# Optimization experiments

Hardware: AMD Instinct MI355X
Metric: run time of the kernel (lower is better)

Reference implementation:

```python
import jax, jax.numpy as jnp
import numpy as np

B, N, C, H = 4, 1024, 768, 12
D = C // H  # head_dim = 64


def setup_inputs() -> dict:
    key = jax.random.key(0)
    ks = jax.random.split(key, 16)
    def lin(k, fan_in, fan_out):
        # torch Linear init: U(-1/sqrt(fan_in), 1/sqrt(fan_in)); stored as [in, out]
        bound = 1.0 / np.sqrt(fan_in)
        kw, kb = jax.random.split(k)
        W = jax.random.uniform(kw, (fan_in, fan_out), minval=-bound, maxval=bound, dtype=jnp.float32)
        b = jax.random.uniform(kb, (fan_out,), minval=-bound, maxval=bound, dtype=jnp.float32)
        return W, b
    Wq, bq = lin(ks[0], C, C)
    Wk, bk = lin(ks[1], C, C)
    Wv, bv = lin(ks[2], C, C)
    Wo, bo = lin(ks[3], C, C)
    Wd1, bd1 = lin(ks[4], 1, 16)
    Wd2, bd2 = lin(ks[5], 16, H)
    x = jax.random.normal(ks[6], (B, N, C), dtype=jnp.float32)
    coords = jax.random.uniform(ks[7], (B, N, 2), dtype=jnp.float32)
    return {"x": x, "coords": coords,
            "Wq": Wq, "bq": bq, "Wk": Wk, "bk": bk, "Wv": Wv, "bv": bv,
            "Wo": Wo, "bo": bo, "Wd1": Wd1, "bd1": bd1, "Wd2": Wd2, "bd2": bd2}


def reference(x, coords, Wq, bq, Wk, bk, Wv, bv, Wo, bo, Wd1, bd1, Wd2, bd2):
    scale = D ** (-0.5)
    # projections -> [B, H, N, D]
    def heads(t):
        return t.reshape(B, N, H, D).transpose(0, 2, 1, 3)
    q = heads(x @ Wq + bq)
    k = heads(x @ Wk + bk)
    v = heads(x @ Wv + bv)
    # content scores [B, H, N, N]
    content = jnp.einsum('bhid,bhjd->bhij', q, k) * scale
    # pairwise distances [B, N, N, 1]
    diff = coords[:, :, None, :] - coords[:, None, :, :]
    dist = jnp.sqrt(jnp.sum(diff * diff, axis=-1, keepdims=True) + 1e-6)
    # distance MLP: 1 -> 16 -> H, then permute to [B, H, N, N]
    hbias = jax.nn.relu(dist @ Wd1 + bd1)
    spatial = (hbias @ Wd2 + bd2).transpose(0, 3, 1, 2)
    attn = jax.nn.softmax(content + spatial, axis=-1)
    out = jnp.einsum('bhij,bhjd->bhid', attn, v)
    out = out.transpose(0, 2, 1, 3).reshape(B, N, C)
    out = out @ Wo + bo
    return out, attn
```

## Files before the change

kernel.cpp:

```cpp
#include <hip/hip_runtime.h>
#include <cstddef>
#include <cstdint>

#define Bc 4
#define Nc 1024
#define Cc 768
#define Hc 12
#define Dc 64
#define BHc 48
#define QKV_ELEMS ((size_t)Bc * Nc * Cc)

typedef __attribute__((ext_vector_type(4))) unsigned int u32x4;
typedef __attribute__((ext_vector_type(2))) unsigned int u32x2;
typedef __attribute__((ext_vector_type(8))) short s16x8;
typedef __attribute__((ext_vector_type(8))) _Float16 h16x8;
typedef __attribute__((ext_vector_type(4))) float fx4;
typedef __attribute__((ext_vector_type(2))) float fx2;

union Frag { u32x4 u; s16x8 s; h16x8 f16; unsigned short h[8]; };

__device__ inline unsigned short f2bf(float x) {
    union { float f; uint32_t u; } c; c.f = x;
    return (unsigned short)((c.u + 0x7FFFu + ((c.u >> 16) & 1u)) >> 16);
}
__device__ inline float bf2f(unsigned short b) {
    union { uint32_t u; float f; } c; c.u = ((uint32_t)b) << 16;
    return c.f;
}
__device__ inline void split8(const float* v, u32x4& hi, u32x4& lo) {
    Frag fh, fl;
    #pragma unroll
    for (int e = 0; e < 8; ++e) {
        const unsigned short hb = f2bf(v[e]);
        fh.h[e] = hb;
        fl.h[e] = f2bf(v[e] - bf2f(hb));
    }
    hi = fh.u; lo = fl.u;
}
__device__ inline void split8h(const float* v, u32x4& hi, u32x4& lo) {
    Frag fh, fl;
    #pragma unroll
    for (int e = 0; e < 8; ++e) {
        const _Float16 hb = (_Float16)v[e];
        fh.f16[e] = hb;
        fl.f16[e] = (_Float16)(v[e] - (float)hb);
    }
    hi = fh.u; lo = fl.u;
}

__global__ __launch_bounds__(256) void prep_w_kernel(
    const float* __restrict__ Wq, const float* __restrict__ Wk,
    const float* __restrict__ Wv, const float* __restrict__ Wo,
    unsigned short* __restrict__ Thi, unsigned short* __restrict__ Tlo)
{
    __shared__ float scr[64 * 65];
    const int mat = blockIdx.z;
    const float* W = (mat == 0) ? Wq : (mat == 1) ? Wk : (mat == 2) ? Wv : Wo;
    const int k0 = blockIdx.y * 64, n0 = blockIdx.x * 64;
    const int tid = threadIdx.x;

    #pragma unroll
    for (int it = 0; it < 4; ++it) {
        const int lin = tid + it * 256;
        const int r = lin >> 4, c4 = (lin & 15) << 2;
        const fx4 v = *(const fx4*)&W[(size_t)(k0 + r) * 768 + n0 + c4];
        scr[r * 65 + c4 + 0] = v[0]; scr[r * 65 + c4 + 1] = v[1];
        scr[r * 65 + c4 + 2] = v[2]; scr[r * 65 + c4 + 3] = v[3];
    }
    __syncthreads();
    unsigned short* th = Thi + (size_t)mat * 768 * 768;
    unsigned short* tl = Tlo + (size_t)mat * 768 * 768;
    #pragma unroll
    for (int it = 0; it < 16; ++it) {
        const int lin = tid + it * 256;
        const int n = lin >> 6, kq = lin & 63;
        const float val = scr[kq * 65 + n];
        const size_t o = (size_t)(n0 + n) * 768 + k0 + kq;
        const unsigned short hb = f2bf(val);
        th[o] = hb;
        tl[o] = f2bf(val - bf2f(hb));
    }
}

__global__ __launch_bounds__(256) void prep_tables_kernel(
    const float* __restrict__ Wd1, const float* __restrict__ bd1,
    const float* __restrict__ Wd2, const float* __restrict__ bd2,
    float* __restrict__ abPack, unsigned char* __restrict__ lut)
{
    __shared__ float w1s[16], b1s[16], kn[16];
    __shared__ int rank[16];
    const int tid = threadIdx.x;
    if (tid < 16) {
        const float w1 = Wd1[tid], b1 = bd1[tid];
        w1s[tid] = w1; b1s[tid] = b1;
        kn[tid] = (w1 != 0.0f) ? (-b1 / w1) : INFINITY;
    }
    __syncthreads();
    if (tid < 16) {
        int rk = 0;
        for (int u = 0; u < 16; ++u) {
            const float ku = kn[u], km = kn[tid];
            if (ku < km || (ku == km && u < tid)) ++rk;
        }
        rank[tid] = rk;
    }
    __syncthreads();
    if (tid < 17 * 12) {
        const int s = tid / 12, h = tid % 12;
        float a = 0.0f, be = bd2[h];
        for (int u = 0; u < 16; ++u) {
            const float w1 = w1s[u], b1 = b1s[u];
            bool act;
            if (w1 > 0.0f)      act = (rank[u] < s);
            else if (w1 < 0.0f) act = (rank[u] >= s);
            else                act = (b1 > 0.0f);
            if (act) {
                const float w2 = Wd2[u * 12 + h];
                a  += w2 * w1;
                be += w2 * b1;
            }
        }
        abPack[tid * 2 + 0] = a;
        abPack[tid * 2 + 1] = be;
    }
    for (int b = tid; b < 2048; b += 256) {
        const float rep = (b + 0.5f) * (1.41422f / 2048.0f);
        int cnt = 0;
        for (int t = 0; t < 16; ++t) cnt += (rep > kn[t]) ? 1 : 0;
        lut[b] = (unsigned char)cnt;
    }
}

__global__ __launch_bounds__(256) void split_x_kernel(
    const float* __restrict__ x, unsigned short* __restrict__ xhi,
    unsigned short* __restrict__ xlo)
{
    const size_t t = (size_t)blockIdx.x * 256 + threadIdx.x;
    float vv[8];
    const fx4 a = *(const fx4*)&x[t * 8];
    const fx4 b = *(const fx4*)&x[t * 8 + 4];
    vv[0]=a[0]; vv[1]=a[1]; vv[2]=a[2]; vv[3]=a[3];
    vv[4]=b[0]; vv[5]=b[1]; vv[6]=b[2]; vv[7]=b[3];
    u32x4 hi, lo; split8(vv, hi, lo);
    *(u32x4*)&xhi[t * 8] = hi;
    *(u32x4*)&xlo[t * 8] = lo;
}

struct SmemG { u32x4 ah[512]; u32x4 al[512]; u32x4 bh[512]; u32x4 bl[512]; };
struct SmemT { float scr[64 * 68]; };
union SmemU { SmemG g; SmemT t; };

template<int OMODE>
__global__ __launch_bounds__(256) void gemm_mfma_kernel(
    const unsigned short* __restrict__ Ahi, const unsigned short* __restrict__ Alo,
    const unsigned short* __restrict__ Bhi, const unsigned short* __restrict__ Blo,
    const float* __restrict__ bias,
    float* __restrict__ outF,
    unsigned short* __restrict__ Ohi, unsigned short* __restrict__ Olo)
{
    __shared__ SmemU sm;
    const int tid = threadIdx.x;
    const int w = tid >> 6, L = tid & 63;
    const int Lr = L & 15, Lg = L >> 4;
    const int m0 = blockIdx.y * 64, n0 = blockIdx.x * 64;

    fx4 acc[2][2] = {};

    for (int kk = 0; kk < 768; kk += 64) {
        #pragma unroll
        for (int it = 0; it < 2; ++it) {
            const int slot = tid + it * 256;
            const int s = slot >> 6, l = slot & 63;
            const int row = m0 + ((s >> 1) << 4) + (l & 15);
            const int kb = kk + ((s & 1) << 5) + ((l >> 4) << 3);
            sm.g.ah[slot] = *(const u32x4*)&Ahi[(size_t)row * 768 + kb];
            sm.g.al[slot] = *(const u32x4*)&Alo[(size_t)row * 768 + kb];
            const int col = n0 + ((s >> 1) << 4) + (l & 15);
            sm.g.bh[slot] = *(const u32x4*)&Bhi[(size_t)col * 768 + kb];
            sm.g.bl[slot] = *(const u32x4*)&Blo[(size_t)col * 768 + kb];
        }
        __syncthreads();
        #pragma unroll
        for (int kc = 0; kc < 2; ++kc) {
            Frag ah[2], al[2], bh[2], bl[2];
            #pragma unroll
            for (int mm = 0; mm < 2; ++mm) {
                const int rg = (w >> 1) * 2 + mm;
                ah[mm].u = sm.g.ah[(rg * 2 + kc) * 64 + L];
                al[mm].u = sm.g.al[(rg * 2 + kc) * 64 + L];
            }
            #pragma unroll
            for (int nn = 0; nn < 2; ++nn) {
                const int cg = (w & 1) * 2 + nn;
                bh[nn].u = sm.g.bh[(cg * 2 + kc) * 64 + L];
                bl[nn].u = sm.g.bl[(cg * 2 + kc) * 64 + L];
            }
            #pragma unroll
            for (int mm = 0; mm < 2; ++mm)
                #pragma unroll
                for (int nn = 0; nn < 2; ++nn) {
                    acc[mm][nn] = __builtin_amdgcn_mfma_f32_16x16x32_bf16(ah[mm].s, bh[nn].s, acc[mm][nn], 0, 0, 0);
                    acc[mm][nn] = __builtin_amdgcn_mfma_f32_16x16x32_bf16(ah[mm].s, bl[nn].s, acc[mm][nn], 0, 0, 0);
                    acc[mm][nn] = __builtin_amdgcn_mfma_f32_16x16x32_bf16(al[mm].s, bh[nn].s, acc[mm][nn], 0, 0, 0);
                }
        }
        __syncthreads();
    }

    #pragma unroll
    for (int mm = 0; mm < 2; ++mm) {
        const int rl = (w >> 1) * 32 + mm * 16 + Lg * 4;
        #pragma unroll
        for (int nn = 0; nn < 2; ++nn) {
            const int cl = (w & 1) * 32 + nn * 16 + Lr;
            const float bs = bias[n0 + cl];
            #pragma unroll
            for (int r = 0; r < 4; ++r)
                sm.t.scr[(rl + r) * 68 + cl] = acc[mm][nn][r] + bs;
        }
    }
    __syncthreads();

    if (OMODE == 0) {
        const int h = n0 >> 6;
        #pragma unroll
        for (int it = 0; it < 2; ++it) {
            const int t = tid + it * 256;
            const int r = t >> 3, d0 = (t & 7) << 3;
            float vv[8];
            #pragma unroll
            for (int e = 0; e < 8; ++e) vv[e] = sm.t.scr[r * 68 + d0 + e];
            u32x4 hi, lo; split8(vv, hi, lo);
            const int rg = m0 + r, b = rg >> 10, nloc = rg & 1023;
            const size_t o = (((size_t)(b * Hc + h) * Nc + nloc) << 6) + d0;
            *(u32x4*)&Ohi[o] = hi;
            *(u32x4*)&Olo[o] = lo;
        }
    } else if (OMODE == 1) {
        const int b = m0 >> 10, h = n0 >> 6, nbase = m0 & 1023;
        #pragma unroll
        for (int it = 0; it < 2; ++it) {
            const int t = tid + it * 256;
            const int dd = t >> 3, j0 = (t & 7) << 3;
            float vv[8];
            #pragma unroll
            for (int e = 0; e < 8; ++e) vv[e] = sm.t.scr[(j0 + e) * 68 + dd];
            u32x4 hi, lo; split8h(vv, hi, lo);
            const size_t o = (size_t)((b * Hc + h) * Dc + dd) * Nc + nbase + j0;
            *(u32x4*)&Ohi[o] = hi;
            *(u32x4*)&Olo[o] = lo;
        }
    } else {
        #pragma unroll
        for (int it = 0; it < 4; ++it) {
            const int lin = tid + it * 256;
            const int r = lin >> 4, c4 = (lin & 15) << 2;
            const fx4 v = *(const fx4*)&sm.t.scr[r * 68 + c4];
            *(fx4*)&outF[(size_t)(m0 + r) * 768 + n0 + c4] = v;
        }
    }
}

union PvSmem {
    struct { u32x4 vh[512]; u32x4 vl[512]; } v;
    float scr[64 * 68];
};

__global__ __launch_bounds__(256) void attn_fused_kernel(
    const unsigned short* __restrict__ qhi, const unsigned short* __restrict__ qlo,
    const unsigned short* __restrict__ khi, const unsigned short* __restrict__ klo,
    const unsigned short* __restrict__ vThi, const unsigned short* __restrict__ vTlo,
    const float* __restrict__ coords,
    const float* __restrict__ abPack, const unsigned char* __restrict__ lutg,
    float* __restrict__ attn,
    unsigned short* __restrict__ Hphi, unsigned short* __restrict__ Hplo)
{
    __shared__ PvSmem sm;
    __shared__ char escr[4 * 2048];
    __shared__ fx2 cjs[1024];
    __shared__ unsigned char luts[2048];
    __shared__ fx2 abt[17];

    const int tid = threadIdx.x;
    const int w = tid >> 6, L = tid & 63;
    const int Lr = L & 15, Lg = L >> 4;
    const int bh = blockIdx.y, b = bh / Hc, h = bh % Hc;
    const int i0 = blockIdx.x * 64;
    const int i = i0 + w * 16 + Lr;
    const int Lg4 = Lg * 4;

    if (tid < 17) abt[tid] = ((const fx2*)abPack)[tid * Hc + h];
    #pragma unroll
    for (int t = tid; t < 512; t += 256)
        ((uint32_t*)luts)[t] = ((const uint32_t*)lutg)[t];
    #pragma unroll
    for (int t = tid; t < 1024; t += 256)
        cjs[t] = *(const fx2*)&coords[((size_t)b * Nc + t) * 2];

    Frag qh[2], ql[2];
    #pragma unroll
    for (int kc = 0; kc < 2; ++kc) {
        const size_t o = ((size_t)bh * Nc + i) * 64 + kc * 32 + Lg * 8;
        qh[kc].u = *(const u32x4*)&qhi[o];
        ql[kc].u = *(const u32x4*)&qlo[o];
    }
    const fx2 ci = *(const fx2*)&coords[((size_t)b * Nc + i) * 2];
    __syncthreads();

    Frag ef[16][2];
    float m_t[16];
    float m_r = -INFINITY, l_r = 0.f;

    #pragma unroll
    for (int jt = 0; jt < 16; ++jt) {
        const int jbase = jt * 64;

        fx4 acc[4] = {};
        #pragma unroll
        for (int kc = 0; kc < 2; ++kc) {
            Frag kh[4], kl[4];
            #pragma unroll
            for (int cg = 0; cg < 4; ++cg) {
                const size_t o = ((size_t)bh * Nc + jbase + cg * 16 + Lr) * 64 + kc * 32 + Lg * 8;
                kh[cg].u = *(const u32x4*)&khi[o];
                kl[cg].u = *(const u32x4*)&klo[o];
            }
            #pragma unroll
            for (int cg = 0; cg < 4; ++cg) {
                acc[cg] = __builtin_amdgcn_mfma_f32_16x16x32_bf16(kh[cg].s, qh[kc].s, acc[cg], 0, 0, 0);
                acc[cg] = __builtin_amdgcn_mfma_f32_16x16x32_bf16(kl[cg].s, qh[kc].s, acc[cg], 0, 0, 0);
                acc[cg] = __builtin_amdgcn_mfma_f32_16x16x32_bf16(kh[cg].s, ql[kc].s, acc[cg], 0, 0, 0);
            }
        }

        float sv[16];
        #pragma unroll
        for (int cg = 0; cg < 4; ++cg) {
            #pragma unroll
            for (int r = 0; r < 4; ++r) {
                const fx2 cj = cjs[jbase + cg * 16 + Lg4 + r];
                const float dx = ci[0] - cj[0], dy = ci[1] - cj[1];
                const float dist = sqrtf(fmaf(dx, dx, fmaf(dy, dy, 1e-6f)));
                int bin = (int)(dist * (2048.0f / 1.41422f));
                bin = (bin > 2047) ? 2047 : bin;
                const fx2 ab = abt[luts[bin]];
                sv[cg * 4 + r] = fmaf(acc[cg][r], 0.125f, fmaf(ab[0], dist, ab[1]));
            }
        }

        float tm = sv[0];
        #pragma unroll
        for (int e = 1; e < 16; ++e) tm = fmaxf(tm, sv[e]);
        tm = fmaxf(tm, __shfl_xor(tm, 16));
        tm = fmaxf(tm, __shfl_xor(tm, 32));
        m_t[jt] = tm;

        float ts = 0.f;
        #pragma unroll
        for (int e = 0; e < 16; ++e) { sv[e] = __expf(sv[e] - tm); ts += sv[e]; }
        ts += __shfl_xor(ts, 16);
        ts += __shfl_xor(ts, 32);

        #pragma unroll
        for (int p = 0; p < 2; ++p) {
            Frag f;
            #pragma unroll
            for (int r = 0; r < 4; ++r) {
                f.f16[r]     = (_Float16)sv[(2 * p) * 4 + r];
                f.f16[4 + r] = (_Float16)sv[(2 * p + 1) * 4 + r];
            }
            ef[jt][p] = f;
        }

        const float mnew = fmaxf(m_r, tm);
        l_r = l_r * __expf(m_r - mnew) + ts * __expf(tm - mnew);
        m_r = mnew;
    }

    const float m_row = m_r;
    const float il = 1.0f / l_r;

    char* ebase = escr + w * 2048;
    fx4 oacc[4] = {};
    const size_t arow = ((size_t)bh * Nc + i) * Nc;

    #pragma unroll
    for (int jt = 0; jt < 16; ++jt) {
        const int jbase = jt * 64;
        #pragma unroll
        for (int it = 0; it < 2; ++it) {
            const int s = tid + it * 256;
            const int l = s & 63;
            const int dd = ((s >> 7) << 4) + (l & 15);
            const int jo = jbase + ((s >> 6) & 1) * 32 + ((l >> 4) << 3);
            const size_t off = ((size_t)bh * Dc + dd) * Nc + jo;
            sm.v.vh[s] = *(const u32x4*)&vThi[off];
            sm.v.vl[s] = *(const u32x4*)&vTlo[off];
        }

        #pragma unroll
        for (int p = 0; p < 2; ++p) {
            const Frag f = ef[jt][p];
            u32x2 lo2, hi2;
            lo2[0] = f.u[0]; lo2[1] = f.u[1];
            hi2[0] = f.u[2]; hi2[1] = f.u[3];
            const int j0 = (2 * p) * 16 + Lg4;
            const int j1 = (2 * p + 1) * 16 + Lg4;
            *(u32x2*)(ebase + ((Lr * 128 + j0 * 2) ^ ((Lr & 7) << 4))) = lo2;
            *(u32x2*)(ebase + ((Lr * 128 + j1 * 2) ^ ((Lr & 7) << 4))) = hi2;
        }
        __syncthreads();

        const float fscale = __expf(m_t[jt] - m_row) * il;
        const _Float16 fh = (_Float16)fscale;

        #pragma unroll
        for (int kc = 0; kc < 2; ++kc) {
            Frag eA;
            eA.u = *(u32x4*)(ebase + ((Lr * 128 + (kc * 32 + Lg * 8) * 2) ^ ((Lr & 7) << 4)));
            float pf[8];
            #pragma unroll
            for (int e = 0; e < 8; ++e) pf[e] = (float)eA.f16[e] * fscale;
            fx4 w0, w1;
            w0[0]=pf[0]; w0[1]=pf[1]; w0[2]=pf[2]; w0[3]=pf[3];
            w1[0]=pf[4]; w1[1]=pf[5]; w1[2]=pf[6]; w1[3]=pf[7];
            float* ap = &attn[arow + jbase + kc * 32 + Lg * 8];
            *(fx4*)ap = w0;
            *(fx4*)(ap + 4) = w1;
            Frag pa;
            pa.f16 = eA.f16 * fh;
            #pragma unroll
            for (int dg = 0; dg < 4; ++dg) {
                Frag vh, vl;
                vh.u = sm.v.vh[(dg * 2 + kc) * 64 + L];
                vl.u = sm.v.vl[(dg * 2 + kc) * 64 + L];
                oacc[dg] = __builtin_amdgcn_mfma_f32_16x16x32_f16(pa.f16, vh.f16, oacc[dg], 0, 0, 0);
                oacc[dg] = __builtin_amdgcn_mfma_f32_16x16x32_f16(pa.f16, vl.f16, oacc[dg], 0, 0, 0);
            }
        }
        __syncthreads();
    }

    #pragma unroll
    for (int dg = 0; dg < 4; ++dg)
        #pragma unroll
        for (int r = 0; r < 4; ++r)
            sm.scr[(w * 16 + Lg * 4 + r) * 68 + dg * 16 + Lr] = oacc[dg][r];
    __syncthreads();

    #pragma unroll
    for (int it = 0; it < 2; ++it) {
        const int lin = tid + it * 256;
        const int row = lin >> 3, d0 = (lin & 7) << 3;
        float vv[8];
        #pragma unroll
        for (int e = 0; e < 8; ++e) vv[e] = sm.scr[row * 68 + d0 + e];
        u32x4 hi, lo; split8(vv, hi, lo);
        const size_t o = ((size_t)b * Nc + i0 + row) * Cc + h * Dc + d0;
        *(u32x4*)&Hphi[o] = hi;
        *(u32x4*)&Hplo[o] = lo;
    }
}

extern "C" void kernel_launch(void* const* d_in, const int* in_sizes, int n_in,
                              void* d_out, int out_size, void* d_ws, size_t ws_size,
                              hipStream_t stream)
{
    (void)in_sizes; (void)n_in; (void)out_size; (void)ws_size;

    const float* x      = (const float*)d_in[0];
    const float* coords = (const float*)d_in[1];
    const float* Wq = (const float*)d_in[2];  const float* bq = (const float*)d_in[3];
    const float* Wk = (const float*)d_in[4];  const float* bk = (const float*)d_in[5];
    const float* Wv = (const float*)d_in[6];  const float* bv = (const float*)d_in[7];
    const float* Wo = (const float*)d_in[8];  const float* bo = (const float*)d_in[9];
    const float* Wd1 = (const float*)d_in[10]; const float* bd1 = (const float*)d_in[11];
    const float* Wd2 = (const float*)d_in[12]; const float* bd2 = (const float*)d_in[13];

    float* out_main = (float*)d_out;
    float* attn     = out_main + QKV_ELEMS;

    uint8_t* wsb = (uint8_t*)d_ws;
    const size_t SZ_BF = (size_t)BHc * Nc * Dc * 2;
    const size_t SZ_W4 = (size_t)4 * 768 * 768 * 2;
    unsigned short* qhi  = (unsigned short*)(wsb + 0 * SZ_BF);
    unsigned short* qlo  = (unsigned short*)(wsb + 1 * SZ_BF);
    unsigned short* khi  = (unsigned short*)(wsb + 2 * SZ_BF);
    unsigned short* klo  = (unsigned short*)(wsb + 3 * SZ_BF);
    unsigned short* vThi = (unsigned short*)(wsb + 4 * SZ_BF);
    unsigned short* vTlo = (unsigned short*)(wsb + 5 * SZ_BF);
    unsigned short* xhi  = (unsigned short*)(wsb + 6 * SZ_BF);
    unsigned short* xlo  = (unsigned short*)(wsb + 7 * SZ_BF);
    unsigned short* Thi  = (unsigned short*)(wsb + 8 * SZ_BF);
    unsigned short* Tlo  = (unsigned short*)(wsb + 8 * SZ_BF + SZ_W4);
    float* abPack = (float*)(wsb + 8 * SZ_BF + 2 * SZ_W4);
    unsigned char* lut = (unsigned char*)(abPack + 17 * 12 * 2);

    prep_w_kernel<<<dim3(12, 12, 4), 256, 0, stream>>>(Wq, Wk, Wv, Wo, Thi, Tlo);
    prep_tables_kernel<<<1, 256, 0, stream>>>(Wd1, bd1, Wd2, bd2, abPack, lut);
    split_x_kernel<<<dim3(1536), 256, 0, stream>>>(x, xhi, xlo);

    dim3 gGemm(12, 64);
    gemm_mfma_kernel<0><<<gGemm, 256, 0, stream>>>(
        xhi, xlo, Thi + (size_t)0 * 768 * 768, Tlo + (size_t)0 * 768 * 768,
        bq, nullptr, qhi, qlo);
    gemm_mfma_kernel<0><<<gGemm, 256, 0, stream>>>(
        xhi, xlo, Thi + (size_t)1 * 768 * 768, Tlo + (size_t)1 * 768 * 768,
        bk, nullptr, khi, klo);
    gemm_mfma_kernel<1><<<gGemm, 256, 0, stream>>>(
        xhi, xlo, Thi + (size_t)2 * 768 * 768, Tlo + (size_t)2 * 768 * 768,
        bv, nullptr, vThi, vTlo);

    attn_fused_kernel<<<dim3(16, 48), 256, 0, stream>>>(
        qhi, qlo, khi, klo, vThi, vTlo, coords, abPack, lut,
        attn, xhi, xlo);

    gemm_mfma_kernel<2><<<gGemm, 256, 0, stream>>>(
        xhi, xlo, Thi + (size_t)3 * 768 * 768, Tlo + (size_t)3 * 768 * 768,
        bo, out_main, nullptr, nullptr);
}
```

Baseline: 462.1 us.

## Merge QKV GEMMs and switch attention to single-pass online softmax with deferred normalization

The three Q/K/V projection launches become one batched launch over a z-dimension. The attention kernel drops its two-pass structure, which held all 16 tiles of fp16 exponentials in registers. It now does a single flash-style online softmax, rescaling the output accumulator per tile and prefetching V for the next tile into registers. Unnormalized fp16 exponentials and per-tile maxima go to a workspace, and a new norm_kernel rescales them into the fp32 attention matrix. This is meant to cut register pressure and raise occupancy, at the cost of an extra fp16 round trip of the N×N scores through global memory and one more launch.

```diff
diff --git a/kernel.cpp b/kernel.cpp
--- a/kernel.cpp
+++ b/kernel.cpp
@@ -18,6 +18,7 @@
 typedef __attribute__((ext_vector_type(2))) float fx2;
 
 union Frag { u32x4 u; s16x8 s; h16x8 f16; unsigned short h[8]; };
+union H4 { u32x2 d; _Float16 h[4]; };
 
 __device__ inline unsigned short f2bf(float x) {
     union { float f; uint32_t u; } c; c.f = x;
@@ -150,13 +151,123 @@
 struct SmemT { float scr[64 * 68]; };
 union SmemU { SmemG g; SmemT t; };
 
+__global__ __launch_bounds__(256) void qkv_kernel(
+    const unsigned short* __restrict__ xhi, const unsigned short* __restrict__ xlo,
+    const unsigned short* __restrict__ Thi, const unsigned short* __restrict__ Tlo,
+    const float* __restrict__ bq, const float* __restrict__ bk,
+    const float* __restrict__ bv,
+    unsigned short* __restrict__ qhi, unsigned short* __restrict__ qlo,
+    unsigned short* __restrict__ khi, unsigned short* __restrict__ klo,
+    unsigned short* __restrict__ vThi, unsigned short* __restrict__ vTlo)
+{
+    __shared__ SmemU sm;
+    const int tid = threadIdx.x;
+    const int w = tid >> 6, L = tid & 63;
+    const int Lr = L & 15, Lg = L >> 4;
+    const int m0 = blockIdx.y * 64, n0 = blockIdx.x * 64;
+    const int mat = blockIdx.z;
+
+    const unsigned short* Bhi = Thi + (size_t)mat * 768 * 768;
+    const unsigned short* Blo = Tlo + (size_t)mat * 768 * 768;
+    const float* bias = (mat == 0) ? bq : (mat == 1) ? bk : bv;
+
+    fx4 acc[2][2] = {};
+
+    for (int kk = 0; kk < 768; kk += 64) {
+        #pragma unroll
+        for (int it = 0; it < 2; ++it) {
+            const int slot = tid + it * 256;
+            const int s = slot >> 6, l = slot & 63;
+            const int row = m0 + ((s >> 1) << 4) + (l & 15);
+            const int kb = kk + ((s & 1) << 5) + ((l >> 4) << 3);
+            sm.g.ah[slot] = *(const u32x4*)&xhi[(size_t)row * 768 + kb];
+            sm.g.al[slot] = *(const u32x4*)&xlo[(size_t)row * 768 + kb];
+            const int col = n0 + ((s >> 1) << 4) + (l & 15);
+            sm.g.bh[slot] = *(const u32x4*)&Bhi[(size_t)col * 768 + kb];
+            sm.g.bl[slot] = *(const u32x4*)&Blo[(size_t)col * 768 + kb];
+        }
+        __syncthreads();
+        #pragma unroll
+        for (int kc = 0; kc < 2; ++kc) {
+            Frag ah[2], al[2], bh[2], bl[2];
+            #pragma unroll
+            for (int mm = 0; mm < 2; ++mm) {
+                const int rg = (w >> 1) * 2 + mm;
+                ah[mm].u = sm.g.ah[(rg * 2 + kc) * 64 + L];
+                al[mm].u = sm.g.al[(rg * 2 + kc) * 64 + L];
+            }
+            #pragma unroll
+            for (int nn = 0; nn < 2; ++nn) {
+                const int cg = (w & 1) * 2 + nn;
+                bh[nn].u = sm.g.bh[(cg * 2 + kc) * 64 + L];
+                bl[nn].u = sm.g.bl[(cg * 2 + kc) * 64 + L];
+            }
+            #pragma unroll
+            for (int mm = 0; mm < 2; ++mm)
+                #pragma unroll
+                for (int nn = 0; nn < 2; ++nn) {
+                    acc[mm][nn] = __builtin_amdgcn_mfma_f32_16x16x32_bf16(ah[mm].s, bh[nn].s, acc[mm][nn], 0, 0, 0);
+                    acc[mm][nn] = __builtin_amdgcn_mfma_f32_16x16x32_bf16(ah[mm].s, bl[nn].s, acc[mm][nn], 0, 0, 0);
+                    acc[mm][nn] = __builtin_amdgcn_mfma_f32_16x16x32_bf16(al[mm].s, bh[nn].s, acc[mm][nn], 0, 0, 0);
+                }
+        }
+        __syncthreads();
+    }
+
+    #pragma unroll
+    for (int mm = 0; mm < 2; ++mm) {
+        const int rl = (w >> 1) * 32 + mm * 16 + Lg * 4;
+        #pragma unroll
+        for (int nn = 0; nn < 2; ++nn) {
+            const int cl = (w & 1) * 32 + nn * 16 + Lr;
+            const float bs = bias[n0 + cl];
+            #pragma unroll
+            for (int r = 0; r < 4; ++r)
+                sm.t.scr[(rl + r) * 68 + cl] = acc[mm][nn][r] + bs;
+        }
+    }
+    __syncthreads();
+
+    if (mat < 2) {
+        unsigned short* Ohi = (mat == 0) ? qhi : khi;
+        unsigned short* Olo = (mat == 0) ? qlo : klo;
+        const int h = n0 >> 6;
+        #pragma unroll
+        for (int it = 0; it < 2; ++it) {
+            const int t = tid + it * 256;
+            const int r = t >> 3, d0 = (t & 7) << 3;
+            float vv[8];
+            #pragma unroll
+            for (int e = 0; e < 8; ++e) vv[e] = sm.t.scr[r * 68 + d0 + e];
+            u32x4 hi, lo; split8(vv, hi, lo);
+            const int rg = m0 + r, b = rg >> 10, nloc = rg & 1023;
+            const size_t o = (((size_t)(b * Hc + h) * Nc + nloc) << 6) + d0;
+            *(u32x4*)&Ohi[o] = hi;
+            *(u32x4*)&Olo[o] = lo;
+        }
+    } else {
+        const int b = m0 >> 10, h = n0 >> 6, nbase = m0 & 1023;
+        #pragma unroll
+        for (int it = 0; it < 2; ++it) {
+            const int t = tid + it * 256;
+            const int dd = t >> 3, j0 = (t & 7) << 3;
+            float vv[8];
+            #pragma unroll
+            for (int e = 0; e < 8; ++e) vv[e] = sm.t.scr[(j0 + e) * 68 + dd];
+            u32x4 hi, lo; split8h(vv, hi, lo);
+            const size_t o = (size_t)((b * Hc + h) * Dc + dd) * Nc + nbase + j0;
+            *(u32x4*)&vThi[o] = hi;
+            *(u32x4*)&vTlo[o] = lo;
+        }
+    }
+}
+
 template<int OMODE>
 __global__ __launch_bounds__(256) void gemm_mfma_kernel(
     const unsigned short* __restrict__ Ahi, const unsigned short* __restrict__ Alo,
     const unsigned short* __restrict__ Bhi, const unsigned short* __restrict__ Blo,
     const float* __restrict__ bias,
-    float* __restrict__ outF,
-    unsigned short* __restrict__ Ohi, unsigned short* __restrict__ Olo)
+    float* __restrict__ outF)
 {
     __shared__ SmemU sm;
     const int tid = threadIdx.x;
@@ -221,62 +332,31 @@
     }
     __syncthreads();
 
-    if (OMODE == 0) {
-        const int h = n0 >> 6;
-        #pragma unroll
-        for (int it = 0; it < 2; ++it) {
-            const int t = tid + it * 256;
-            const int r = t >> 3, d0 = (t & 7) << 3;
-            float vv[8];
-            #pragma unroll
-            for (int e = 0; e < 8; ++e) vv[e] = sm.t.scr[r * 68 + d0 + e];
-            u32x4 hi, lo; split8(vv, hi, lo);
-            const int rg = m0 + r, b = rg >> 10, nloc = rg & 1023;
-            const size_t o = (((size_t)(b * Hc + h) * Nc + nloc) << 6) + d0;
-            *(u32x4*)&Ohi[o] = hi;
-            *(u32x4*)&Olo[o] = lo;
-        }
-    } else if (OMODE == 1) {
-        const int b = m0 >> 10, h = n0 >> 6, nbase = m0 & 1023;
-        #pragma unroll
-        for (int it = 0; it < 2; ++it) {
-            const int t = tid + it * 256;
-            const int dd = t >> 3, j0 = (t & 7) << 3;
-            float vv[8];
-            #pragma unroll
-            for (int e = 0; e < 8; ++e) vv[e] = sm.t.scr[(j0 + e) * 68 + dd];
-            u32x4 hi, lo; split8h(vv, hi, lo);
-            const size_t o = (size_t)((b * Hc + h) * Dc + dd) * Nc + nbase + j0;
-            *(u32x4*)&Ohi[o] = hi;
-            *(u32x4*)&Olo[o] = lo;
-        }
-    } else {
-        #pragma unroll
-        for (int it = 0; it < 4; ++it) {
-            const int lin = tid + it * 256;
-            const int r = lin >> 4, c4 = (lin & 15) << 2;
-            const fx4 v = *(const fx4*)&sm.t.scr[r * 68 + c4];
-            *(fx4*)&outF[(size_t)(m0 + r) * 768 + n0 + c4] = v;
-        }
-    }
-}
-
-union PvSmem {
-    struct { u32x4 vh[512]; u32x4 vl[512]; } v;
+    #pragma unroll
+    for (int it = 0; it < 4; ++it) {
+        const int lin = tid + it * 256;
+        const int r = lin >> 4, c4 = (lin & 15) << 2;
+        const fx4 v = *(const fx4*)&sm.t.scr[r * 68 + c4];
+        *(fx4*)&outF[(size_t)(m0 + r) * 768 + n0 + c4] = v;
+    }
+}
+
+union FlashSmem {
+    struct { u32x4 vh[512]; u32x4 vl[512]; char escr[4 * 2304]; } p;
     float scr[64 * 68];
 };
 
-__global__ __launch_bounds__(256) void attn_fused_kernel(
+__global__ __launch_bounds__(256) void attn_flash_kernel(
     const unsigned short* __restrict__ qhi, const unsigned short* __restrict__ qlo,
     const unsigned short* __restrict__ khi, const unsigned short* __restrict__ klo,
     const unsigned short* __restrict__ vThi, const unsigned short* __restrict__ vTlo,
     const float* __restrict__ coords,
     const float* __restrict__ abPack, const unsigned char* __restrict__ lutg,
-    float* __restrict__ attn,
+    unsigned short* __restrict__ e_ws, float* __restrict__ mT,
+    float* __restrict__ mlfin,
     unsigned short* __restrict__ Hphi, unsigned short* __restrict__ Hplo)
 {
-    __shared__ PvSmem sm;
-    __shared__ char escr[4 * 2048];
+    __shared__ FlashSmem sm;
     __shared__ fx2 cjs[1024];
     __shared__ unsigned char luts[2048];
     __shared__ fx2 abt[17];
@@ -290,10 +370,8 @@
     const int Lg4 = Lg * 4;
 
     if (tid < 17) abt[tid] = ((const fx2*)abPack)[tid * Hc + h];
-    #pragma unroll
     for (int t = tid; t < 512; t += 256)
         ((uint32_t*)luts)[t] = ((const uint32_t*)lutg)[t];
-    #pragma unroll
     for (int t = tid; t < 1024; t += 256)
         cjs[t] = *(const fx2*)&coords[((size_t)b * Nc + t) * 2];
 
@@ -307,13 +385,24 @@
     const fx2 ci = *(const fx2*)&coords[((size_t)b * Nc + i) * 2];
     __syncthreads();
 
-    Frag ef[16][2];
-    float m_t[16];
+    char* eb = sm.p.escr + w * 2304;
+    fx4 oacc[4] = {};
     float m_r = -INFINITY, l_r = 0.f;
 
-    #pragma unroll
     for (int jt = 0; jt < 16; ++jt) {
         const int jbase = jt * 64;
+
+        u32x4 vsh[2], vsl[2];
+        #pragma unroll
+        for (int it = 0; it < 2; ++it) {
+            const int s = tid + it * 256;
+            const int l = s & 63;
+            const int dd = ((s >> 7) << 4) + (l & 15);
+            const int jo = jbase + ((s >> 6) & 1) * 32 + ((l >> 4) << 3);
+            const size_t off = ((size_t)bh * Dc + dd) * Nc + jo;
+            vsh[it] = *(const u32x4*)&vThi[off];
+            vsl[it] = *(const u32x4*)&vTlo[off];
+        }
 
         fx4 acc[4] = {};
         #pragma unroll
@@ -353,7 +442,6 @@
         for (int e = 1; e < 16; ++e) tm = fmaxf(tm, sv[e]);
         tm = fmaxf(tm, __shfl_xor(tm, 16));
         tm = fmaxf(tm, __shfl_xor(tm, 32));
-        m_t[jt] = tm;
 
         float ts = 0.f;
         #pragma unroll
@@ -361,91 +449,69 @@
         ts += __shfl_xor(ts, 16);
         ts += __shfl_xor(ts, 32);
 
-        #pragma unroll
-        for (int p = 0; p < 2; ++p) {
-            Frag f;
-            #pragma unroll
-            for (int r = 0; r < 4; ++r) {
-                f.f16[r]     = (_Float16)sv[(2 * p) * 4 + r];
-                f.f16[4 + r] = (_Float16)sv[(2 * p + 1) * 4 + r];
-            }
-            ef[jt][p] = f;
-        }
-
-        const float mnew = fmaxf(m_r, tm);
-        l_r = l_r * __expf(m_r - mnew) + ts * __expf(tm - mnew);
-        m_r = mnew;
-    }
-
-    const float m_row = m_r;
-    const float il = 1.0f / l_r;
-
-    char* ebase = escr + w * 2048;
-    fx4 oacc[4] = {};
-    const size_t arow = ((size_t)bh * Nc + i) * Nc;
-
-    #pragma unroll
-    for (int jt = 0; jt < 16; ++jt) {
-        const int jbase = jt * 64;
+        if (Lg == 0) mT[((size_t)bh * Nc + i) * 16 + jt] = tm;
+
+        __syncthreads();
         #pragma unroll
         for (int it = 0; it < 2; ++it) {
             const int s = tid + it * 256;
-            const int l = s & 63;
-            const int dd = ((s >> 7) << 4) + (l & 15);
-            const int jo = jbase + ((s >> 6) & 1) * 32 + ((l >> 4) << 3);
-            const size_t off = ((size_t)bh * Dc + dd) * Nc + jo;
-            sm.v.vh[s] = *(const u32x4*)&vThi[off];
-            sm.v.vl[s] = *(const u32x4*)&vTlo[off];
-        }
-
-        #pragma unroll
-        for (int p = 0; p < 2; ++p) {
-            const Frag f = ef[jt][p];
-            u32x2 lo2, hi2;
-            lo2[0] = f.u[0]; lo2[1] = f.u[1];
-            hi2[0] = f.u[2]; hi2[1] = f.u[3];
-            const int j0 = (2 * p) * 16 + Lg4;
-            const int j1 = (2 * p + 1) * 16 + Lg4;
-            *(u32x2*)(ebase + ((Lr * 128 + j0 * 2) ^ ((Lr & 7) << 4))) = lo2;
-            *(u32x2*)(ebase + ((Lr * 128 + j1 * 2) ^ ((Lr & 7) << 4))) = hi2;
+            sm.p.vh[s] = vsh[it];
+            sm.p.vl[s] = vsl[it];
+        }
+        #pragma unroll
+        for (int cg = 0; cg < 4; ++cg) {
+            H4 pk;
+            #pragma unroll
+            for (int r = 0; r < 4; ++r) pk.h[r] = (_Float16)sv[cg * 4 + r];
+            *(u32x2*)(eb + Lr * 144 + (cg * 4 + Lg) * 8) = pk.d;
         }
         __syncthreads();
 
-        const float fscale = __expf(m_t[jt] - m_row) * il;
-        const _Float16 fh = (_Float16)fscale;
-
+        const float mnew = fmaxf(m_r, tm);
+        const float facc = __expf(m_r - mnew);
+        const float ftile = __expf(tm - mnew);
+        l_r = l_r * facc + ts * ftile;
+        m_r = mnew;
+        #pragma unroll
+        for (int r = 0; r < 4; ++r) {
+            const float fr = __shfl(facc, Lg4 + r);
+            #pragma unroll
+            for (int dg = 0; dg < 4; ++dg) oacc[dg][r] *= fr;
+        }
+        const _Float16 fh = (_Float16)ftile;
+
+        const size_t ebase_g = (size_t)((bh * 16 + jt) * 2) * 32768 + (size_t)i * 32 + Lg * 8;
         #pragma unroll
         for (int kc = 0; kc < 2; ++kc) {
             Frag eA;
-            eA.u = *(u32x4*)(ebase + ((Lr * 128 + (kc * 32 + Lg * 8) * 2) ^ ((Lr & 7) << 4)));
-            float pf[8];
-            #pragma unroll
-            for (int e = 0; e < 8; ++e) pf[e] = (float)eA.f16[e] * fscale;
-            fx4 w0, w1;
-            w0[0]=pf[0]; w0[1]=pf[1]; w0[2]=pf[2]; w0[3]=pf[3];
-            w1[0]=pf[4]; w1[1]=pf[5]; w1[2]=pf[6]; w1[3]=pf[7];
-            float* ap = &attn[arow + jbase + kc * 32 + Lg * 8];
-            *(fx4*)ap = w0;
-            *(fx4*)(ap + 4) = w1;
+            eA.u = *(const u32x4*)(eb + Lr * 144 + kc * 64 + Lg * 16);
+            *(u32x4*)&e_ws[ebase_g + (size_t)kc * 32768] = eA.u;
             Frag pa;
             pa.f16 = eA.f16 * fh;
             #pragma unroll
             for (int dg = 0; dg < 4; ++dg) {
-                Frag vh, vl;
-                vh.u = sm.v.vh[(dg * 2 + kc) * 64 + L];
-                vl.u = sm.v.vl[(dg * 2 + kc) * 64 + L];
-                oacc[dg] = __builtin_amdgcn_mfma_f32_16x16x32_f16(pa.f16, vh.f16, oacc[dg], 0, 0, 0);
-                oacc[dg] = __builtin_amdgcn_mfma_f32_16x16x32_f16(pa.f16, vl.f16, oacc[dg], 0, 0, 0);
-            }
-        }
-        __syncthreads();
-    }
-
+                Frag vh_, vl_;
+                vh_.u = sm.p.vh[(dg * 2 + kc) * 64 + L];
+                vl_.u = sm.p.vl[(dg * 2 + kc) * 64 + L];
+                oacc[dg] = __builtin_amdgcn_mfma_f32_16x16x32_f16(pa.f16, vh_.f16, oacc[dg], 0, 0, 0);
+                oacc[dg] = __builtin_amdgcn_mfma_f32_16x16x32_f16(pa.f16, vl_.f16, oacc[dg], 0, 0, 0);
+            }
+        }
+    }
+
+    const float il = 1.0f / l_r;
+    if (Lg == 0) *(fx2*)&mlfin[2 * ((size_t)bh * Nc + i)] = fx2{m_r, il};
+
+    float il4[4];
+    #pragma unroll
+    for (int r = 0; r < 4; ++r) il4[r] = __shfl(il, Lg4 + r);
+
+    __syncthreads();
     #pragma unroll
     for (int dg = 0; dg < 4; ++dg)
         #pragma unroll
         for (int r = 0; r < 4; ++r)
-            sm.scr[(w * 16 + Lg * 4 + r) * 68 + dg * 16 + Lr] = oacc[dg][r];
+            sm.scr[(w * 16 + Lg4 + r) * 68 + dg * 16 + Lr] = oacc[dg][r] * il4[r];
     __syncthreads();
 
     #pragma unroll
@@ -459,6 +525,39 @@
         const size_t o = ((size_t)b * Nc + i0 + row) * Cc + h * Dc + d0;
         *(u32x4*)&Hphi[o] = hi;
         *(u32x4*)&Hplo[o] = lo;
+    }
+}
+
+__global__ __launch_bounds__(256) void norm_kernel(
+    const unsigned short* __restrict__ e_ws,
+    const float* __restrict__ mT, const float* __restrict__ mlfin,
+    float* __restrict__ attn)
+{
+    const size_t t = (size_t)blockIdx.x * 256 + threadIdx.x;
+    const int blk = (int)(t >> 10);
+    const int i = (int)(t & 1023);
+    const int bh = blk >> 5;
+    const int jt = (blk >> 1) & 15;
+    const int kc = blk & 1;
+    const size_t row = (size_t)bh * Nc + i;
+
+    const fx2 mf = *(const fx2*)&mlfin[2 * row];
+    const float mt = mT[row * 16 + jt];
+    const float f = __expf(mt - mf[0]) * mf[1];
+
+    const unsigned short* ep = &e_ws[(size_t)blk * 32768 + (size_t)i * 32];
+    float* ap = &attn[row * Nc + jt * 64 + kc * 32];
+    #pragma unroll
+    for (int c = 0; c < 4; ++c) {
+        Frag ev;
+        ev.u = *(const u32x4*)&ep[c * 8];
+        fx4 o0, o1;
+        o0[0] = (float)ev.f16[0] * f; o0[1] = (float)ev.f16[1] * f;
+        o0[2] = (float)ev.f16[2] * f; o0[3] = (float)ev.f16[3] * f;
+        o1[0] = (float)ev.f16[4] * f; o1[1] = (float)ev.f16[5] * f;
+        o1[2] = (float)ev.f16[6] * f; o1[3] = (float)ev.f16[7] * f;
+        *(fx4*)&ap[c * 8] = o0;
+        *(fx4*)&ap[c * 8 + 4] = o1;
     }
 }
 
@@ -493,29 +592,28 @@
     unsigned short* xlo  = (unsigned short*)(wsb + 7 * SZ_BF);
     unsigned short* Thi  = (unsigned short*)(wsb + 8 * SZ_BF);
     unsigned short* Tlo  = (unsigned short*)(wsb + 8 * SZ_BF + SZ_W4);
-    float* abPack = (float*)(wsb + 8 * SZ_BF + 2 * SZ_W4);
-    unsigned char* lut = (unsigned char*)(abPack + 17 * 12 * 2);
+    uint8_t* base8 = wsb + 8 * SZ_BF + 2 * SZ_W4;
+    float* abPack = (float*)base8;
+    unsigned char* lut = (unsigned char*)(base8 + 4096);
+    float* mT    = (float*)(base8 + 8192);
+    float* mlfin = mT + (size_t)BHc * Nc * 16;
+    unsigned short* e_ws = (unsigned short*)(mlfin + (size_t)BHc * Nc * 2);
 
     prep_w_kernel<<<dim3(12, 12, 4), 256, 0, stream>>>(Wq, Wk, Wv, Wo, Thi, Tlo);
     prep_tables_kernel<<<1, 256, 0, stream>>>(Wd1, bd1, Wd2, bd2, abPack, lut);
     split_x_kernel<<<dim3(1536), 256, 0, stream>>>(x, xhi, xlo);
 
-    dim3 gGemm(12, 64);
-    gemm_mfma_kernel<0><<<gGemm, 256, 0, stream>>>(
-        xhi, xlo, Thi + (size_t)0 * 768 * 768, Tlo + (size_t)0 * 768 * 768,
-        bq, nullptr, qhi, qlo);
-    gemm_mfma_kernel<0><<<gGemm, 256, 0, stream>>>(
-        xhi, xlo, Thi + (size_t)1 * 768 * 768, Tlo + (size_t)1 * 768 * 768,
-        bk, nullptr, khi, klo);
-    gemm_mfma_kernel<1><<<gGemm, 256, 0, stream>>>(
-        xhi, xlo, Thi + (size_t)2 * 768 * 768, Tlo + (size_t)2 * 768 * 768,
-        bv, nullptr, vThi, vTlo);
-
-    attn_fused_kernel<<<dim3(16, 48), 256, 0, stream>>>(
+    qkv_kernel<<<dim3(12, 64, 3), 256, 0, stream>>>(
+        xhi, xlo, Thi, Tlo, bq, bk, bv,
+        qhi, qlo, khi, klo, vThi, vTlo);
+
+    attn_flash_kernel<<<dim3(16, 48), 256, 0, stream>>>(
         qhi, qlo, khi, klo, vThi, vTlo, coords, abPack, lut,
-        attn, xhi, xlo);
-
-    gemm_mfma_kernel<2><<<gGemm, 256, 0, stream>>>(
+        e_ws, mT, mlfin, xhi, xlo);
+
+    norm_kernel<<<dim3(6144), 256, 0, stream>>>(e_ws, mT, mlfin, attn);
+
+    gemm_mfma_kernel<2><<<dim3(12, 64), 256, 0, stream>>>(
         xhi, xlo, Thi + (size_t)3 * 768 * 768, Tlo + (size_t)3 * 768 * 768,
-        bo, out_main, nullptr, nullptr);
-}
+        bo, out_main);
+}
```

New measurement: 424.8 us. 1.09x faster.
